# Kernel optimization log

Measured on AMD Instinct MI355X. Metric: run time of the kernel, lower is better.

## Reference

```python
import jax, jax.numpy as jnp
import numpy as np

N = 50000          # nodes
E = 1_600_000      # edges (avg degree 32)
IN = 128           # in_channels
H = 64             # hidden_channels = middle_channel
OUT = 40           # out_channels
ALPHA = 0.8
NO_GRAD_STEPS = 3  # iter_nums = (4, 1) -> 3 no-grad + 1 grad step
GRAD_STEPS = 1
LN_EPS = 1e-5


def setup_inputs() -> dict:
    key = jax.random.key(0)
    ks = jax.random.split(key, 8)
    x = jax.random.normal(ks[0], (N, IN), jnp.float32)
    edge_index = jax.random.randint(ks[1], (2, E), 0, N, dtype=jnp.int64)
    # per-node symmetric-normalization factor, strictly positive (deg^-1/2-like)
    norm_factor = jax.random.uniform(ks[2], (N, 1), jnp.float32, 0.1, 1.0)
    kaiming = lambda k, shape, fan_in: jax.random.normal(k, shape, jnp.float32) * np.float32(np.sqrt(2.0 / fan_in))
    We = kaiming(ks[3], (H, IN), IN)      # extractor weight
    be = jnp.zeros((H,), jnp.float32)
    W = kaiming(ks[4], (H, H), H)         # Implicit_Func.W (no bias)
    U = kaiming(ks[5], (H, H), H)         # Implicit_Func.U
    bU = jnp.zeros((H,), jnp.float32)
    gamma = jnp.ones((H,), jnp.float32)   # LayerNorm affine
    beta = jnp.zeros((H,), jnp.float32)
    Wlast = jax.random.normal(ks[6], (OUT, H), jnp.float32) * np.float32(np.sqrt(2.0 / (H + OUT)))  # xavier
    blast = jnp.zeros((OUT,), jnp.float32)
    return dict(x=x, edge_index=edge_index, norm_factor=norm_factor,
                We=We, be=be, W=W, U=U, bU=bU, gamma=gamma, beta=beta,
                Wlast=Wlast, blast=blast)


def _layernorm(m, gamma, beta):
    mu = jnp.mean(m, axis=-1, keepdims=True)
    var = jnp.mean((m - mu) ** 2, axis=-1, keepdims=True)
    return gamma * (m - mu) * jax.lax.rsqrt(var + LN_EPS) + beta


def _step(z, xU, nf, row, col, W, gamma, beta):
    # WzUx = norm_factor * (W z + degree * U x)   (xU precomputed as degree*(Ux+b))
    h = nf * (z @ W.T + xU)                       # [N, H]
    m = jnp.tanh(h[row] - h[col])                 # gather-diff + act, [E, H]
    m = _layernorm(m, gamma, beta)
    # scatter_add back to nodes with norm weighting
    a = (jax.ops.segment_sum(m * nf[row], row, num_segments=N)
         - jax.ops.segment_sum(m * nf[col], col, num_segments=N))  # [N, H]
    new_z = -(a @ W)                              # F.linear(a, W.t()) = a @ W
    return ALPHA * new_z + (1.0 - ALPHA) * z


def reference(x, edge_index, norm_factor, We, be, W, U, bU, gamma, beta, Wlast, blast):
    row, col = edge_index[0], edge_index[1]
    xh = x @ We.T + be                            # extractor, [N, H]
    degree = 1.0 / norm_factor
    degree = jnp.where(jnp.isinf(degree), 0.0, degree)
    xU = degree * (xh @ U.T + bU)                 # constant across iterations
    z = jnp.zeros_like(xh)
    for _ in range(NO_GRAD_STEPS):
        z = _step(z, xU, norm_factor, row, col, W, gamma, beta)
    z = jax.lax.stop_gradient(z)
    for _ in range(GRAD_STEPS):
        z = _step(z, xU, norm_factor, row, col, W, gamma, beta)
    z = norm_factor * z + xh                      # rescale + residual
    return z @ Wlast.T + blast                    # linear head, [N, OUT]
```

## Files before the change

### kernel.cpp

```cpp
#include <hip/hip_runtime.h>
#include <hip/hip_bf16.h>

#define NN   50000
#define EE   1600000
#define INC  128
#define HH   64
#define OUTC 40
#define ALPHA 0.8f
#define LN_EPS 1e-5f
#define CAP  128
#define KTANH 2.8853900817779268f

typedef int v4i_t __attribute__((ext_vector_type(4)));
typedef _Float16 h8 __attribute__((ext_vector_type(8)));
typedef __fp16 hv2 __attribute__((ext_vector_type(2)));
typedef float f32x4 __attribute__((ext_vector_type(4)));
typedef int i32x2 __attribute__((ext_vector_type(2)));
typedef int i32x4 __attribute__((ext_vector_type(4)));

__device__ float llvm_amdgcn_raw_buffer_load_fp32(v4i_t srsrc, int voffset,
                                                  int soffset, int glc_slc)
    __asm("llvm.amdgcn.raw.buffer.load.f32");

__device__ __forceinline__ float rl63(float x) {
    return __int_as_float(__builtin_amdgcn_readlane(__float_as_int(x), 63));
}
#define RLF(X, L) __int_as_float(__builtin_amdgcn_readlane(__float_as_int(X), (L)))

__device__ __forceinline__ float fast_tanh_pre(float xs) {
    float e = __builtin_amdgcn_exp2f(xs);
    float u = __builtin_amdgcn_rcpf(1.0f + e);
    return __builtin_fmaf(-2.0f, u, 1.0f);
}

__device__ __forceinline__ h8 mk8(i32x2 a, i32x2 b) {
    i32x4 t = {a.x, a.y, b.x, b.y};
    return __builtin_bit_cast(h8, t);
}

struct TileAcc { float a0, a1, a2, a3, sc; };

#define TRRD(D, OFF)                                                           \
    asm volatile("ds_read_b64_tr_b16 %0, %1 offset:" OFF                       \
                 : "=v"(D) : "v"(trv))

template <bool GUARD>
__device__ __forceinline__ void tile16(
        TileAcc& A, float hn, int nrem,
        float h0, float h1, float h2, float h3,
        float h4, float h5, float h6, float h7,
        float h8v, float h9, float h10, float h11,
        float h12, float h13, float h14, float h15,
        char* wp, int trv, h8 ones) {
    float d0 = fast_tanh_pre(hn - h0);
    float d1 = fast_tanh_pre(hn - h1);
    float d2 = fast_tanh_pre(hn - h2);
    float d3 = fast_tanh_pre(hn - h3);
    float d4 = fast_tanh_pre(hn - h4);
    float d5 = fast_tanh_pre(hn - h5);
    float d6 = fast_tanh_pre(hn - h6);
    float d7 = fast_tanh_pre(hn - h7);
    float d8 = fast_tanh_pre(hn - h8v);
    float d9 = fast_tanh_pre(hn - h9);
    float d10 = fast_tanh_pre(hn - h10);
    float d11 = fast_tanh_pre(hn - h11);
    float d12 = fast_tanh_pre(hn - h12);
    float d13 = fast_tanh_pre(hn - h13);
    float d14 = fast_tanh_pre(hn - h14);
    float d15 = fast_tanh_pre(hn - h15);
    if (GUARD) {
        if (!(0 < nrem))  d0 = 0.f;
        if (!(1 < nrem))  d1 = 0.f;
        if (!(2 < nrem))  d2 = 0.f;
        if (!(3 < nrem))  d3 = 0.f;
        if (!(4 < nrem))  d4 = 0.f;
        if (!(5 < nrem))  d5 = 0.f;
        if (!(6 < nrem))  d6 = 0.f;
        if (!(7 < nrem))  d7 = 0.f;
        if (!(8 < nrem))  d8 = 0.f;
        if (!(9 < nrem))  d9 = 0.f;
        if (!(10 < nrem)) d10 = 0.f;
        if (!(11 < nrem)) d11 = 0.f;
        if (!(12 < nrem)) d12 = 0.f;
        if (!(13 < nrem)) d13 = 0.f;
        if (!(14 < nrem)) d14 = 0.f;
        if (!(15 < nrem)) d15 = 0.f;
    }
    hv2 p0 = __builtin_amdgcn_cvt_pkrtz(d0, d1);
    hv2 p1 = __builtin_amdgcn_cvt_pkrtz(d2, d3);
    hv2 p2 = __builtin_amdgcn_cvt_pkrtz(d4, d5);
    hv2 p3 = __builtin_amdgcn_cvt_pkrtz(d6, d7);
    hv2 p4 = __builtin_amdgcn_cvt_pkrtz(d8, d9);
    hv2 p5 = __builtin_amdgcn_cvt_pkrtz(d10, d11);
    hv2 p6 = __builtin_amdgcn_cvt_pkrtz(d12, d13);
    hv2 p7 = __builtin_amdgcn_cvt_pkrtz(d14, d15);
    hv2 q0 = p0 * p0, q1 = p1 * p1, q2 = p2 * p2, q3 = p3 * p3;
    hv2 q4 = p4 * p4, q5 = p5 * p5, q6 = p6 * p6, q7 = p7 * p7;
#define BC(X) __builtin_bit_cast(int, X)
    i32x4 wA = {BC(p0), BC(p1), BC(p2), BC(p3)};
    i32x4 wB = {BC(p4), BC(p5), BC(p6), BC(p7)};
    i32x4 wC = {BC(q0), BC(q1), BC(q2), BC(q3)};
    i32x4 wD = {BC(q4), BC(q5), BC(q6), BC(q7)};
#undef BC
    *(i32x4*)(wp)        = wA;
    *(i32x4*)(wp + 16)   = wB;
    *(i32x4*)(wp + 2048) = wC;
    *(i32x4*)(wp + 2064) = wD;
    asm volatile("" ::: "memory");
    i32x2 r0, r1, r2, r3, r4, r5, r6, r7;
    TRRD(r0, "0");    TRRD(r1, "128");
    TRRD(r2, "1024"); TRRD(r3, "1152");
    TRRD(r4, "2048"); TRRD(r5, "2176");
    TRRD(r6, "3072"); TRRD(r7, "3200");
    asm volatile("s_waitcnt lgkmcnt(0)"
                 : "+v"(r0), "+v"(r1), "+v"(r2), "+v"(r3),
                   "+v"(r4), "+v"(r5), "+v"(r6), "+v"(r7) :: "memory");
    h8 a0 = mk8(r0, r1), a1 = mk8(r2, r3);
    h8 b0 = mk8(r4, r5), b1 = mk8(r6, r7);
    f32x4 s1 = {0.f, 0.f, 0.f, 0.f}, s2 = {0.f, 0.f, 0.f, 0.f};
    s1 = __builtin_amdgcn_mfma_f32_16x16x32_f16(a0, ones, s1, 0, 0, 0);
    s1 = __builtin_amdgcn_mfma_f32_16x16x32_f16(a1, ones, s1, 0, 0, 0);
    s2 = __builtin_amdgcn_mfma_f32_16x16x32_f16(b0, ones, s2, 0, 0, 0);
    s2 = __builtin_amdgcn_mfma_f32_16x16x32_f16(b1, ones, s2, 0, 0, 0);
    float mu0 = s1[0] * 0.015625f;
    float mu1 = s1[1] * 0.015625f;
    float mu2 = s1[2] * 0.015625f;
    float mu3 = s1[3] * 0.015625f;
    float v0 = __builtin_fmaf(s2[0], 0.015625f, __builtin_fmaf(-mu0, mu0, LN_EPS));
    float v1 = __builtin_fmaf(s2[1], 0.015625f, __builtin_fmaf(-mu1, mu1, LN_EPS));
    float v2 = __builtin_fmaf(s2[2], 0.015625f, __builtin_fmaf(-mu2, mu2, LN_EPS));
    float v3 = __builtin_fmaf(s2[3], 0.015625f, __builtin_fmaf(-mu3, mu3, LN_EPS));
    float rs0 = __frsqrt_rn(v0);
    float rs1 = __frsqrt_rn(v1);
    float rs2 = __frsqrt_rn(v2);
    float rs3 = __frsqrt_rn(v3);
    A.sc += __builtin_fmaf(rs0, mu0,
            __builtin_fmaf(rs1, mu1,
            __builtin_fmaf(rs2, mu2, rs3 * mu3)));
    A.a0 = __builtin_fmaf(RLF(rs0, 0), d0, A.a0);
    A.a1 = __builtin_fmaf(RLF(rs1, 0), d1, A.a1);
    A.a2 = __builtin_fmaf(RLF(rs2, 0), d2, A.a2);
    A.a3 = __builtin_fmaf(RLF(rs3, 0), d3, A.a3);
    A.a0 = __builtin_fmaf(RLF(rs0, 16), d4, A.a0);
    A.a1 = __builtin_fmaf(RLF(rs1, 16), d5, A.a1);
    A.a2 = __builtin_fmaf(RLF(rs2, 16), d6, A.a2);
    A.a3 = __builtin_fmaf(RLF(rs3, 16), d7, A.a3);
    A.a0 = __builtin_fmaf(RLF(rs0, 32), d8, A.a0);
    A.a1 = __builtin_fmaf(RLF(rs1, 32), d9, A.a1);
    A.a2 = __builtin_fmaf(RLF(rs2, 32), d10, A.a2);
    A.a3 = __builtin_fmaf(RLF(rs3, 32), d11, A.a3);
    A.a0 = __builtin_fmaf(RLF(rs0, 48), d12, A.a0);
    A.a1 = __builtin_fmaf(RLF(rs1, 48), d13, A.a1);
    A.a2 = __builtin_fmaf(RLF(rs2, 48), d14, A.a2);
    A.a3 = __builtin_fmaf(RLF(rs3, 48), d15, A.a3);
}

__global__ __launch_bounds__(256) void csr_build(const int* __restrict__ ei,
                                                 int* __restrict__ cnt,
                                                 unsigned short* __restrict__ adj) {
    int i = blockIdx.x * 256 + threadIdx.x;
    if (i >= 2 * EE) return;
    int node = ei[i];
    int other, add;
    if (i >= EE) { other = ei[i - EE]; add = 0x10001; }
    else         { other = ei[i + EE]; add = 1; }
    int r = atomicAdd(&cnt[node], add) & 0xffff;
    if (r < CAP) adj[node * CAP + r] = (unsigned short)other;
}

__global__ __launch_bounds__(256) void make_G(const float* __restrict__ W,
                                              float* __restrict__ G) {
    __shared__ float Ws[64 * 64];
    for (int t = threadIdx.x; t < 64 * 64; t += 256) Ws[t] = W[t];
    __syncthreads();
    int t = blockIdx.x * 256 + threadIdx.x;
    int i = t >> 6, j = t & 63;
    float acc = 0.f;
#pragma unroll 8
    for (int k = 0; k < 64; ++k) acc += Ws[i * 64 + k] * Ws[j * 64 + k];
    G[t] = acc;
}

__global__ __launch_bounds__(256) void extractor(
        const float* __restrict__ x, const float* __restrict__ nf,
        const float* __restrict__ We, const float* __restrict__ be,
        const float* __restrict__ U,  const float* __restrict__ bU,
        float* __restrict__ xh, float* __restrict__ xU, float* __restrict__ h0) {
    __shared__ float WeT[INC * HH];
    __shared__ float UT[HH * HH];
    __shared__ float beS[HH], bUS[HH];
    __shared__ float xs[4][INC];
    __shared__ float xhs[4][HH];

    for (int t = threadIdx.x; t < INC * HH; t += 256) {
        int j = t >> 7, k = t & 127;
        WeT[k * 64 + j] = We[t];
    }
    for (int t = threadIdx.x; t < HH * HH; t += 256) {
        int j = t >> 6, k = t & 63;
        UT[k * 64 + j] = U[t];
    }
    if (threadIdx.x < 64) { beS[threadIdx.x] = be[threadIdx.x]; bUS[threadIdx.x] = bU[threadIdx.x]; }
    __syncthreads();

    int lane = threadIdx.x & 63;
    int wv   = threadIdx.x >> 6;

    for (int n0 = blockIdx.x * 4; n0 < NN; n0 += gridDim.x * 4) {
        int n = n0 + wv;
        bool valid = n < NN;
        if (valid) {
            xs[wv][lane]      = x[(size_t)n * INC + lane];
            xs[wv][lane + 64] = x[(size_t)n * INC + lane + 64];
        }
        __syncthreads();
        float acc = beS[lane];
        if (valid) {
#pragma unroll 8
            for (int k = 0; k < INC; ++k) acc += xs[wv][k] * WeT[k * 64 + lane];
            xh[n * 64 + lane] = acc;
            xhs[wv][lane] = acc;
        }
        __syncthreads();
        if (valid) {
            float acc2 = bUS[lane];
#pragma unroll 8
            for (int k = 0; k < HH; ++k) acc2 += xhs[wv][k] * UT[k * 64 + lane];
            h0[n * 64 + lane] = KTANH * acc2;
            xU[n * 64 + lane] = acc2 / nf[n];
        }
        __syncthreads();
    }
}

#define HV(P) P##0, P##1, P##2, P##3, P##4, P##5, P##6, P##7,                 \
              P##8, P##9, P##10, P##11, P##12, P##13, P##14, P##15

#define EVX(EV, J)                                                             \
    ((((RL((EV), (J) >> 1)) >> (((J) & 1) << 4)) & 0xffff) << 8)

#define G16P(P, EV, J)                                                         \
    do {                                                                       \
        P##0  = GATH(EVX(EV, (J) + 0));  P##1  = GATH(EVX(EV, (J) + 1));       \
        P##2  = GATH(EVX(EV, (J) + 2));  P##3  = GATH(EVX(EV, (J) + 3));       \
        P##4  = GATH(EVX(EV, (J) + 4));  P##5  = GATH(EVX(EV, (J) + 5));       \
        P##6  = GATH(EVX(EV, (J) + 6));  P##7  = GATH(EVX(EV, (J) + 7));       \
        P##8  = GATH(EVX(EV, (J) + 8));  P##9  = GATH(EVX(EV, (J) + 9));       \
        P##10 = GATH(EVX(EV, (J) + 10)); P##11 = GATH(EVX(EV, (J) + 11));      \
        P##12 = GATH(EVX(EV, (J) + 12)); P##13 = GATH(EVX(EV, (J) + 13));      \
        P##14 = GATH(EVX(EV, (J) + 14)); P##15 = GATH(EVX(EV, (J) + 15));      \
    } while (0)

#define NPREF(P)                                                               \
    do { if (morenode) { G16P(P, evN, 0); } } while (0)

#define TILF(BUF) tile16<false>(A, hn, 16, HV(BUF), wp, trv, ones)
#define TILG(BUF, NR) tile16<true>(A, hn, (NR), HV(BUF), wp, trv, ones)

__global__ __launch_bounds__(256) void fused_step(
        const int* __restrict__ adjI,
        const int* __restrict__ cnt,
        const float* __restrict__ hcur, float* __restrict__ hnxt,
        const float* __restrict__ nf, const float* __restrict__ gamma,
        const float* __restrict__ beta, const float* __restrict__ Gm,
        const float* __restrict__ xU,
        float* __restrict__ y, float* __restrict__ s, int first, int last) {
    __shared__ float Gs[64 * 64];
    __shared__ __align__(16) _Float16 dt[4][2048];
    for (int t = threadIdx.x; t < 64 * 64; t += 256) Gs[t] = Gm[t];
    __syncthreads();

    const int lane = threadIdx.x & 63, wv = threadIdx.x >> 6;
    const float g = gamma[lane], b = beta[lane];

    v4i_t hsr;
    {
        unsigned long long up = (unsigned long long)(uintptr_t)hcur;
        hsr.x = (int)(unsigned)(up & 0xffffffffull);
        hsr.y = (int)(unsigned)(up >> 32);
        hsr.z = NN * HH * 4;
        hsr.w = 0x00020000;
    }
    const int lane4 = lane << 2;
#define GATH(e) llvm_amdgcn_raw_buffer_load_fp32(hsr, lane4, (e), 0)
#define RL(v, i) __builtin_amdgcn_readlane((v), (i))

    _Float16* tb = &dt[wv][0];
    char* wp = (char*)tb + lane * 32;
    const unsigned tbb = (unsigned)(uintptr_t)tb;
    const int trv = (int)(tbb + ((lane >> 4) << 8) + ((lane & 15) << 3));
    const h8 ones = {(_Float16)1.f, (_Float16)1.f, (_Float16)1.f, (_Float16)1.f,
                     (_Float16)1.f, (_Float16)1.f, (_Float16)1.f, (_Float16)1.f};

    const int NW = 2048 * 4;
    int n = blockIdx.x * 4 + wv;
    int cP   = __builtin_amdgcn_readfirstlane(cnt[n]);
    int deg  = cP & 0xffff;  if (deg > CAP) deg = CAP;
    int sgm  = (cP & 0xffff) - 2 * ((int)((unsigned)cP >> 16));
    int evl  = adjI[n * (CAP / 2) + lane];
    float hn = hcur[(size_t)n * 64 + lane];
    float hA0, hA1, hA2, hA3, hA4, hA5, hA6, hA7;
    float hA8, hA9, hA10, hA11, hA12, hA13, hA14, hA15;
    float hB0, hB1, hB2, hB3, hB4, hB5, hB6, hB7;
    float hB8, hB9, hB10, hB11, hB12, hB13, hB14, hB15;
    G16P(hA, evl, 0);

    for (;;) {
        const int nxt = n + NW;
        const bool morenode = nxt < NN;
        int cN = 0, evN = 0;
        float hnN = 0.f;
        if (morenode) {
            cN  = __builtin_amdgcn_readfirstlane(cnt[nxt]);
            evN = adjI[nxt * (CAP / 2) + lane];
            hnN = hcur[(size_t)nxt * 64 + lane];
        }
        TileAcc A = {0.f, 0.f, 0.f, 0.f, 0.f};

        if (deg > 0) {
            const int nt = (deg + 15) >> 4;
            if (nt > 1) { G16P(hB, evl, 16); } else { NPREF(hB); }
            if (nt == 1) { TILG(hA, deg); }
            else {
                TILF(hA);
                if (nt > 2) { G16P(hA, evl, 32); } else { NPREF(hA); }
                if (nt == 2) { TILG(hB, deg - 16); }
                else {
                    TILF(hB);
                    if (nt > 3) { G16P(hB, evl, 48); } else { NPREF(hB); }
                    if (nt == 3) { TILG(hA, deg - 32); }
                    else {
                        TILF(hA);
                        if (nt > 4) { G16P(hA, evl, 64); } else { NPREF(hA); }
                        if (nt == 4) { TILG(hB, deg - 48); }
                        else {
                            TILF(hB);
                            if (nt > 5) { G16P(hB, evl, 80); } else { NPREF(hB); }
                            if (nt == 5) { TILG(hA, deg - 64); }
                            else {
                                TILF(hA);
                                if (nt > 6) { G16P(hA, evl, 96); } else { NPREF(hA); }
                                if (nt == 6) { TILG(hB, deg - 80); }
                                else {
                                    TILF(hB);
                                    if (nt > 7) { G16P(hB, evl, 112); } else { NPREF(hB); }
                                    if (nt == 7) { TILG(hA, deg - 96); }
                                    else {
                                        TILF(hA);
                                        NPREF(hA);
                                        TILG(hB, deg - 112);
                                    }
                                }
                            }
                        }
                    }
                }
            }
            if (nt & 1) {
                hA0 = hB0;  hA1 = hB1;  hA2 = hB2;  hA3 = hB3;
                hA4 = hB4;  hA5 = hB5;  hA6 = hB6;  hA7 = hB7;
                hA8 = hB8;  hA9 = hB9;  hA10 = hB10; hA11 = hB11;
                hA12 = hB12; hA13 = hB13; hA14 = hB14; hA15 = hB15;
            }
        } else {
            NPREF(hA);
        }

        float scp = A.sc;
        asm volatile(
            "s_nop 1\n\t"
            "v_add_f32_dpp %0, %0, %0 row_bcast:15 row_mask:0xa bank_mask:0xf bound_ctrl:0\n\t"
            "s_nop 1\n\t"
            "v_add_f32_dpp %0, %0, %0 row_bcast:31 row_mask:0xc bank_mask:0xf bound_ctrl:0"
            : "+v"(scp));
        const float accM = ((A.a0 + A.a1) + (A.a2 + A.a3)) - rl63(scp);
        const float nfn = nf[n];
        const float av  = nfn * __builtin_fmaf(g, accM, b * (float)sgm);

        float p = 0.f;
        const int avi = __float_as_int(av);
#pragma unroll
        for (int k = 0; k < 64; ++k) {
            float ak = __int_as_float(RL(avi, k));
            p = __builtin_fmaf(ak, Gs[k * 64 + lane], p);
        }

        float yprev = 0.f, sprev = 0.f;
        if (!first) {
            yprev = y[n * 64 + lane];
            sprev = s[n * 64 + lane];
        }
        const float yv = -ALPHA * p + (1.0f - ALPHA) * yprev;
        y[n * 64 + lane] = yv;
        s[n * 64 + lane] = (1.0f - ALPHA) * sprev + av;
        if (!last) hnxt[n * 64 + lane] = KTANH * (nfn * (yv + xU[n * 64 + lane]));

        if (!morenode) break;
        n = nxt;
        deg = cN & 0xffff;  if (deg > CAP) deg = CAP;
        sgm = (cN & 0xffff) - 2 * ((int)((unsigned)cN >> 16));
        evl = evN; hn = hnN;
    }
#undef GATH
#undef RL
}

__global__ __launch_bounds__(256) void final_out(
        const float* __restrict__ s, const float* __restrict__ xh,
        const float* __restrict__ nf, const float* __restrict__ W,
        const float* __restrict__ Wlast, const float* __restrict__ blast,
        float* __restrict__ out) {
    __shared__ float Ws[64 * 64];
    __shared__ float WlT[64 * OUTC];
    __shared__ float blS[OUTC];
    __shared__ float ss[4][64];
    __shared__ float zfs[4][64];
    for (int t = threadIdx.x; t < 64 * 64; t += 256) Ws[t] = W[t];
    for (int t = threadIdx.x; t < OUTC * 64; t += 256) {
        int o = t >> 6, j = t & 63;
        WlT[j * OUTC + o] = Wlast[t];
    }
    if (threadIdx.x < OUTC) blS[threadIdx.x] = blast[threadIdx.x];
    __syncthreads();
    int lane = threadIdx.x & 63, wv = threadIdx.x >> 6;
    for (int n0 = blockIdx.x * 4; n0 < NN; n0 += gridDim.x * 4) {
        int n = n0 + wv;
        if (n < NN) ss[wv][lane] = s[n * 64 + lane];
        __syncthreads();
        if (n < NN) {
            float z = 0.f;
#pragma unroll 8
            for (int k = 0; k < 64; ++k) z += ss[wv][k] * Ws[k * 64 + lane];
            z *= -ALPHA;
            zfs[wv][lane] = nf[n] * z + xh[n * 64 + lane];
        }
        __syncthreads();
        if (n < NN && lane < OUTC) {
            float acc = blS[lane];
#pragma unroll 8
            for (int j = 0; j < 64; ++j) acc += zfs[wv][j] * WlT[j * OUTC + lane];
            out[n * OUTC + lane] = acc;
        }
        __syncthreads();
    }
}

extern "C" void kernel_launch(void* const* d_in, const int* in_sizes, int n_in,
                              void* d_out, int out_size, void* d_ws, size_t ws_size,
                              hipStream_t stream) {
    const float* x     = (const float*)d_in[0];
    const int*   ei    = (const int*)  d_in[1];
    const float* nf    = (const float*)d_in[2];
    const float* We    = (const float*)d_in[3];
    const float* be    = (const float*)d_in[4];
    const float* W     = (const float*)d_in[5];
    const float* U     = (const float*)d_in[6];
    const float* bU    = (const float*)d_in[7];
    const float* gamma = (const float*)d_in[8];
    const float* beta  = (const float*)d_in[9];
    const float* Wlast = (const float*)d_in[10];
    const float* blast = (const float*)d_in[11];
    float* out = (float*)d_out;

    char* ws = (char*)d_ws;
    size_t off = 0;
    const size_t NH = (size_t)NN * HH * sizeof(float);
    unsigned short* adj = (unsigned short*)(ws + off);
                                                 off += (size_t)NN * CAP * sizeof(unsigned short) + 256;
    int*   cnt    = (int*)(ws + off);            off += (size_t)NN * sizeof(int);
    float* xh     = (float*)(ws + off);          off += NH;
    float* xU     = (float*)(ws + off);          off += NH;
    float* h0     = (float*)(ws + off);          off += NH;
    float* h1     = (float*)(ws + off);          off += NH;
    float* y      = (float*)(ws + off);          off += NH;
    float* s      = (float*)(ws + off);          off += NH;
    float* G      = (float*)(ws + off);          off += (size_t)HH * HH * sizeof(float);

    (void)hipMemsetAsync(cnt, 0, (size_t)NN * sizeof(int), stream);

    csr_build<<<(2 * EE + 255) / 256, 256, 0, stream>>>(ei, cnt, adj);

    make_G<<<16, 256, 0, stream>>>(W, G);
    extractor<<<2048, 256, 0, stream>>>(x, nf, We, be, U, bU, xh, xU, h0);

    float* hc = h0;
    float* hn = h1;
    for (int t = 0; t < 4; ++t) {
        fused_step<<<2048, 256, 0, stream>>>((const int*)adj, cnt, hc, hn, nf,
                                             gamma, beta, G, xU, y, s,
                                             t == 0, t == 3);
        float* tmp = hc; hc = hn; hn = tmp;
    }
    final_out<<<2048, 256, 0, stream>>>(s, xh, nf, W, Wlast, blast, out);
}
```

Baseline: 1.083 ms.

## Build adjacency in per-XCD sub-buckets, then compact into per-node lists

Adjacency construction now gives each XCD its own counter and small bucket per node, selected via the hardware XCC id, so atomics from different XCDs no longer contend on the same cache line across dies. Each thread handles one edge and inserts both directions. A second compaction kernel concatenates the eight sub-buckets into the original per-node adjacency layout and packs the combined count word. The cost is an extra kernel, a larger workspace and extra memory traffic, plus a per-XCD capacity of 36 that could drop edges for skewed degree distributions. Neighbor order within each list also changes.

```diff
diff --git a/kernel.cpp b/kernel.cpp
--- a/kernel.cpp
+++ b/kernel.cpp
@@ -9,6 +9,8 @@
 #define ALPHA 0.8f
 #define LN_EPS 1e-5f
 #define CAP  128
+#define CAPS 36
+#define SUBW (8 * CAPS)
 #define KTANH 2.8853900817779268f
 
 typedef int v4i_t __attribute__((ext_vector_type(4)));
@@ -156,16 +158,58 @@
 }
 
 __global__ __launch_bounds__(256) void csr_build(const int* __restrict__ ei,
-                                                 int* __restrict__ cnt,
-                                                 unsigned short* __restrict__ adj) {
-    int i = blockIdx.x * 256 + threadIdx.x;
-    if (i >= 2 * EE) return;
-    int node = ei[i];
-    int other, add;
-    if (i >= EE) { other = ei[i - EE]; add = 0x10001; }
-    else         { other = ei[i + EE]; add = 1; }
-    int r = atomicAdd(&cnt[node], add) & 0xffff;
-    if (r < CAP) adj[node * CAP + r] = (unsigned short)other;
+                                                 int* __restrict__ sub,
+                                                 unsigned short* __restrict__ subadj) {
+    int j = blockIdx.x * 256 + threadIdx.x;
+    if (j >= EE) return;
+    int u = ei[j];
+    int v = ei[j + EE];
+    int xcd;
+    asm("s_getreg_b32 %0, hwreg(HW_REG_XCC_ID)" : "=s"(xcd));
+    int r0 = atomicAdd(&sub[u * 8 + xcd], 1) & 0xffff;
+    if (r0 < CAPS) subadj[(size_t)u * SUBW + xcd * CAPS + r0] = (unsigned short)v;
+    int r1 = atomicAdd(&sub[v * 8 + xcd], 0x10001) & 0xffff;
+    if (r1 < CAPS) subadj[(size_t)v * SUBW + xcd * CAPS + r1] = (unsigned short)u;
+}
+
+__global__ __launch_bounds__(256) void csr_compact(
+        const int* __restrict__ sub, const unsigned short* __restrict__ subadj,
+        int* __restrict__ cnt, unsigned short* __restrict__ adj) {
+    __shared__ int pd[4][8];
+    const int lane = threadIdx.x & 63, wv = threadIdx.x >> 6;
+    for (int n = blockIdx.x * 4 + wv; n < NN; n += gridDim.x * 4) {
+        const int* p = sub + n * 8;
+        int c0 = p[0], c1 = p[1], c2 = p[2], c3 = p[3];
+        int c4 = p[4], c5 = p[5], c6 = p[6], c7 = p[7];
+        if (lane == 0) {
+            int pr = 0, dd;
+#define STEP(S, C)                                                             \
+            dd = (C) & 0xffff; if (dd > CAPS) dd = CAPS;                       \
+            pd[wv][S] = (pr << 16) | dd; pr += dd;
+            STEP(0, c0) STEP(1, c1) STEP(2, c2) STEP(3, c3)
+            STEP(4, c4) STEP(5, c5) STEP(6, c6) STEP(7, c7)
+#undef STEP
+            int degraw = (c0 & 0xffff) + (c1 & 0xffff) + (c2 & 0xffff) +
+                         (c3 & 0xffff) + (c4 & 0xffff) + (c5 & 0xffff) +
+                         (c6 & 0xffff) + (c7 & 0xffff);
+            int ncol = ((unsigned)c0 >> 16) + ((unsigned)c1 >> 16) +
+                       ((unsigned)c2 >> 16) + ((unsigned)c3 >> 16) +
+                       ((unsigned)c4 >> 16) + ((unsigned)c5 >> 16) +
+                       ((unsigned)c6 >> 16) + ((unsigned)c7 >> 16);
+            cnt[n] = (ncol << 16) | degraw;
+        }
+        const int s = lane >> 3;
+        const int pdv = pd[wv][s];
+        const int pre = pdv >> 16, ds = pdv & 0xffff;
+        const unsigned short* src = subadj + (size_t)n * SUBW + s * CAPS;
+        unsigned short* dst = adj + (size_t)n * CAP + pre;
+        const int kb = lane & 7;
+#pragma unroll
+        for (int t = 0; t < 5; ++t) {
+            int k = kb + 8 * t;
+            if (k < CAPS && k < ds && pre + k < CAP) dst[k] = src[k];
+        }
+    }
 }
 
 __global__ __launch_bounds__(256) void make_G(const float* __restrict__ W,
@@ -467,6 +511,9 @@
     const size_t NH = (size_t)NN * HH * sizeof(float);
     unsigned short* adj = (unsigned short*)(ws + off);
                                                  off += (size_t)NN * CAP * sizeof(unsigned short) + 256;
+    unsigned short* subadj = (unsigned short*)(ws + off);
+                                                 off += (size_t)NN * SUBW * sizeof(unsigned short) + 256;
+    int*   sub    = (int*)(ws + off);            off += (size_t)NN * 8 * sizeof(int);
     int*   cnt    = (int*)(ws + off);            off += (size_t)NN * sizeof(int);
     float* xh     = (float*)(ws + off);          off += NH;
     float* xU     = (float*)(ws + off);          off += NH;
@@ -476,9 +523,10 @@
     float* s      = (float*)(ws + off);          off += NH;
     float* G      = (float*)(ws + off);          off += (size_t)HH * HH * sizeof(float);
 
-    (void)hipMemsetAsync(cnt, 0, (size_t)NN * sizeof(int), stream);
-
-    csr_build<<<(2 * EE + 255) / 256, 256, 0, stream>>>(ei, cnt, adj);
+    (void)hipMemsetAsync(sub, 0, (size_t)NN * 8 * sizeof(int), stream);
+
+    csr_build<<<(EE + 255) / 256, 256, 0, stream>>>(ei, sub, subadj);
+    csr_compact<<<2048, 256, 0, stream>>>(sub, subadj, cnt, adj);
 
     make_G<<<16, 256, 0, stream>>>(W, G);
     extractor<<<2048, 256, 0, stream>>>(x, nf, We, be, U, bU, xh, xU, h0);
```

After: 1.099 ms. Within noise of the previous version (+1.5%).
